# Performance work log

Measured on AMD Instinct MI355X. Metric: run time of the kernel, lower is better.

Reference implementation:

```python
import jax, jax.numpy as jnp
import numpy as np

E = 512          # embed_dim
H = 8            # num_heads
FF = 2048        # ff_dim
MAX_LEN = 5000   # DynamicPositionalEncoding max_len
LN_EPS = 1e-5


def _layernorm(x, g, b):
    mu = jnp.mean(x, axis=-1, keepdims=True)
    var = jnp.mean((x - mu) ** 2, axis=-1, keepdims=True)
    return (x - mu) / jnp.sqrt(var + LN_EPS) * g + b


def setup_inputs() -> dict:
    key = jax.random.key(0)
    ks = jax.random.split(key, 12)
    S, B = 2048, 4
    s = 0.02
    return {
        "x": jax.random.normal(ks[0], (S, B, E), dtype=jnp.float32),
        "pos": jnp.zeros((1, MAX_LEN, E), dtype=jnp.float32),  # torch init: zeros Parameter
        "in_proj_w": jax.random.normal(ks[1], (3 * E, E), dtype=jnp.float32) * s,
        "in_proj_b": jnp.zeros((3 * E,), dtype=jnp.float32),
        "out_w": jax.random.normal(ks[2], (E, E), dtype=jnp.float32) * s,
        "out_b": jnp.zeros((E,), dtype=jnp.float32),
        "w1": jax.random.normal(ks[3], (FF, E), dtype=jnp.float32) * s,
        "b1": jnp.zeros((FF,), dtype=jnp.float32),
        "w2": jax.random.normal(ks[4], (E, FF), dtype=jnp.float32) * s,
        "b2": jnp.zeros((E,), dtype=jnp.float32),
        "g1": jnp.ones((E,), dtype=jnp.float32),
        "be1": jnp.zeros((E,), dtype=jnp.float32),
        "g2": jnp.ones((E,), dtype=jnp.float32),
        "be2": jnp.zeros((E,), dtype=jnp.float32),
        "local_window_size": 128,
    }


def reference(x, pos, in_proj_w, in_proj_b, out_w, out_b, w1, b1, w2, b2,
              g1, be1, g2, be2, local_window_size):
    S, B, _ = x.shape
    w = int(local_window_size)
    # quirk of original: pos encoding sliced by x.size(1) == batch, broadcast over seq
    x = x + pos[:, :B, :]

    # additive mask: local window [i-w, i+w] allowed, plus global columns every 2w
    i = jnp.arange(S)[:, None]
    j = jnp.arange(S)[None, :]
    allowed = (jnp.abs(i - j) <= w) | (j % (2 * w) == 0)
    mask = jnp.where(allowed, 0.0, -jnp.inf).astype(x.dtype)  # (S, S)

    # multihead self-attention (torch MHA semantics, seq-first)
    qkv = x @ in_proj_w.T + in_proj_b                 # (S, B, 3E)
    q, k, v = jnp.split(qkv, 3, axis=-1)
    hd = E // H

    def heads(t):  # (S, B, E) -> (B, H, S, hd)
        return t.reshape(S, B, H, hd).transpose(1, 2, 0, 3)

    q, k, v = heads(q), heads(k), heads(v)
    scale = 1.0 / jnp.sqrt(jnp.asarray(hd, x.dtype))
    scores = jnp.einsum("bhqd,bhkd->bhqk", q * scale, k) + mask
    attn = jax.nn.softmax(scores, axis=-1)
    y = jnp.einsum("bhqk,bhkd->bhqd", attn, v)        # (B, H, S, hd)
    y = y.transpose(2, 0, 1, 3).reshape(S, B, E)
    attn_out = y @ out_w.T + out_b

    x = _layernorm(x + attn_out, g1, be1)
    ff = jax.nn.relu(x @ w1.T + b1) @ w2.T + b2
    x = _layernorm(x + ff, g2, be2)
    return x
```

## Files before the change

### kernel.cpp

```cpp
#include <hip/hip_runtime.h>
#include <hip/hip_bf16.h>
#include <math.h>

#define S_LEN 2048
#define B_SZ  4
#define E_DIM 512
#define H_NUM 8
#define HD    64
#define FF_DIM 2048
#define NROWS 8192
#define WIN   128

typedef unsigned short u16;
typedef __bf16 bf16x8 __attribute__((ext_vector_type(8)));
typedef float  f32x4  __attribute__((ext_vector_type(4)));

__device__ __forceinline__ u16 f2bf(float f) {
  union { float f; unsigned u; } v; v.f = f;
  unsigned u = v.u;
  return (u16)((u + 0x7fffu + ((u >> 16) & 1u)) >> 16);
}

__device__ __forceinline__ unsigned cvtpk(float lo, float hi) {
  unsigned r;
  asm("v_cvt_pk_bf16_f32 %0, %1, %2" : "=v"(r) : "v"(lo), "v"(hi));
  return r;
}

__device__ __forceinline__ void gl_lds16(const u16* gp, u16* lp) {
  __builtin_amdgcn_global_load_lds(
      (const __attribute__((address_space(1))) unsigned int*)gp,
      (__attribute__((address_space(3))) unsigned int*)lp, 16, 0, 0);
}

__global__ __launch_bounds__(256) void prep_kernel(
    const float* __restrict__ x, const float* __restrict__ pos,
    float* __restrict__ xp, u16* __restrict__ xpb,
    const float* __restrict__ s0, const float* __restrict__ s1,
    const float* __restrict__ s2, const float* __restrict__ s3,
    u16* __restrict__ d0, u16* __restrict__ d1,
    u16* __restrict__ d2, u16* __restrict__ d3) {
  int i = blockIdx.x * blockDim.x + threadIdx.x;
  if (i < 1048576) {
    float4 xv = ((const float4*)x)[i];
    float4 pv = ((const float4*)pos)[i & 511];
    float4 o;
    o.x = xv.x + pv.x; o.y = xv.y + pv.y; o.z = xv.z + pv.z; o.w = xv.w + pv.w;
    ((float4*)xp)[i] = o;
    ushort4 ob; ob.x = f2bf(o.x); ob.y = f2bf(o.y); ob.z = f2bf(o.z); ob.w = f2bf(o.w);
    ((ushort4*)xpb)[i] = ob;
  } else {
    int j = i - 1048576;
    const int n0 = 196608, n1 = 65536, n2 = 262144;
    const float4* sp; ushort4* dp; int off;
    if (j < n0)                { sp = (const float4*)s0; dp = (ushort4*)d0; off = j; }
    else if (j < n0 + n1)      { sp = (const float4*)s1; dp = (ushort4*)d1; off = j - n0; }
    else if (j < n0 + n1 + n2) { sp = (const float4*)s2; dp = (ushort4*)d2; off = j - n0 - n1; }
    else                       { sp = (const float4*)s3; dp = (ushort4*)d3; off = j - n0 - n1 - n2; }
    float4 v = sp[off];
    ushort4 o; o.x = f2bf(v.x); o.y = f2bf(v.y); o.z = f2bf(v.z); o.w = f2bf(v.w);
    dp[off] = o;
  }
}

#define GBK 64

template <int BN, int GY>
__global__ __launch_bounds__(256) void mfma_gemm(
    const u16* __restrict__ A, const u16* __restrict__ W,
    const float* __restrict__ bias, float* __restrict__ outf,
    u16* __restrict__ outb, int M, int N, int K, int mode,
    u16* __restrict__ qb, u16* __restrict__ kb, u16* __restrict__ vb) {
  constexpr int TJ = BN / 32;
  __shared__ u16 SMEM[2 * 128 * GBK + 2 * BN * GBK];
  u16* As0 = SMEM;
  u16* Bs0 = SMEM + 2 * 128 * GBK;
  int tid = threadIdx.x;
  int lane = tid & 63;
  int w = tid >> 6;
  int lin = blockIdx.y * 64 + blockIdx.x;
  int xcd = lin & 7, slot = lin >> 3;
  int jj = slot % GY;
  int mm = (slot / GY) * 8 + xcd;
  int m0 = mm * 128;
  int j0 = jj * BN;
  int wrow = (w >> 1) * 64;
  int wcol = (w & 1) * (BN / 2);
  int lm = lane & 15;
  int kq = lane >> 4;
  int sw = lm & 7;
  int r8 = lane >> 3;
  int csrc = ((lane & 7) ^ r8) << 3;

  f32x4 acc[4][TJ];
#pragma unroll
  for (int i = 0; i < 4; i++)
#pragma unroll
    for (int j = 0; j < TJ; j++) acc[i][j] = (f32x4){0.f, 0.f, 0.f, 0.f};

  const u16* Ab = A + (size_t)m0 * K;
  const u16* Wb = W + (size_t)j0 * K;

  size_t soff[4];
#pragma unroll
  for (int u = 0; u < 4; u++)
    soff[u] = (size_t)(u * 32 + w * 8 + r8) * K + csrc;

  auto stage = [&](int kt, int pb) {
#pragma unroll
    for (int u = 0; u < 4; u++)
      gl_lds16(&Ab[soff[u] + kt], &As0[pb * 128 * GBK + (u * 4 + w) * 512]);
#pragma unroll
    for (int u = 0; u < TJ; u++)
      gl_lds16(&Wb[soff[u] + kt], &Bs0[pb * BN * GBK + (u * 4 + w) * 512]);
  };

  stage(0, 0);
  int pb = 0;
  for (int kt = 0; kt < K; kt += GBK) {
    __syncthreads();
    if (kt + GBK < K) stage(kt + GBK, pb ^ 1);
#pragma unroll
    for (int k2 = 0; k2 < GBK; k2 += 32) {
      int cc = ((((k2 >> 3) + kq) ^ sw) << 3);
      bf16x8 af[4], bfr[TJ];
#pragma unroll
      for (int t = 0; t < 4; t++)
        af[t] = *(const bf16x8*)&As0[pb * 128 * GBK + (wrow + t * 16 + lm) * GBK + cc];
#pragma unroll
      for (int tj = 0; tj < TJ; tj++)
        bfr[tj] = *(const bf16x8*)&Bs0[pb * BN * GBK + (wcol + tj * 16 + lm) * GBK + cc];
#pragma unroll
      for (int ti = 0; ti < 4; ti++)
#pragma unroll
        for (int tj = 0; tj < TJ; tj++)
          acc[ti][tj] = __builtin_amdgcn_mfma_f32_16x16x32_bf16(
              af[ti], bfr[tj], acc[ti][tj], 0, 0, 0);
    }
    pb ^= 1;
  }

  __syncthreads();
  if (mode == 0) {
    float* Cf = (float*)SMEM;
    constexpr int CF = BN + 4;
#pragma unroll
    for (int p = 0; p < 2; p++) {
      if ((w >> 1) == p) {
#pragma unroll
        for (int tj = 0; tj < TJ; tj++) {
          float bv = bias[j0 + wcol + tj * 16 + lm];
#pragma unroll
          for (int ti = 0; ti < 4; ti++)
#pragma unroll
            for (int r = 0; r < 4; r++)
              Cf[(ti * 16 + kq * 4 + r) * CF + wcol + tj * 16 + lm] =
                  acc[ti][tj][r] + bv;
        }
      }
      __syncthreads();
      constexpr int RC4 = BN / 4;
#pragma unroll
      for (int it = 0; it < 64 * RC4 / 256; it++) {
        int id = it * 256 + tid;
        int row = id / RC4, c4 = (id % RC4) * 4;
        float4 vq = *(float4*)&Cf[row * CF + c4];
        *(float4*)&outf[(size_t)(m0 + p * 64 + row) * N + j0 + c4] = vq;
      }
      __syncthreads();
    }
  } else {
    u16* Cs = (u16*)SMEM;
    constexpr int CS = BN + 8;
#pragma unroll
    for (int tj = 0; tj < TJ; tj++) {
      int colj = j0 + wcol + tj * 16 + lm;
      float bv = bias[colj];
      float qs = (mode == 2 && colj < 512) ? 0.125f : 1.f;
#pragma unroll
      for (int ti = 0; ti < 4; ti++)
#pragma unroll
        for (int r = 0; r < 4; r++) {
          float val = acc[ti][tj][r] + bv;
          if (mode == 1) val = fmaxf(val, 0.f);
          Cs[(wrow + ti * 16 + kq * 4 + r) * CS + wcol + tj * 16 + lm] =
              f2bf(val * qs);
        }
    }
    __syncthreads();
    constexpr int RC8 = BN / 8;
#pragma unroll
    for (int it = 0; it < 128 * RC8 / 256; it++) {
      int id = it * 256 + tid;
      int row = id / RC8, c8 = (id % RC8) * 8;
      uint4 vq = *(uint4*)&Cs[row * CS + c8];
      if (mode == 1) {
        *(uint4*)&outb[(size_t)(m0 + row) * N + j0 + c8] = vq;
      } else {
        int col = j0 + c8;
        int which = col >> 9;
        int e = col & 511;
        int h = e >> 6, d0 = e & 63;
        int m = m0 + row, s = m >> 2, b = m & 3;
        u16* dst = (which == 0) ? qb : (which == 1) ? kb : vb;
        *(uint4*)&dst[((size_t)(b * H_NUM + h) * S_LEN + s) * HD + d0] = vq;
      }
    }
  }
}

__global__ __launch_bounds__(256) void vtrans_kernel(
    const u16* __restrict__ vb, u16* __restrict__ vt) {
  __shared__ u16 T[64 * 72];
  int tid = threadIdx.x;
  int bh = blockIdx.y, sc = blockIdx.x;
  const u16* src = vb + ((size_t)bh * S_LEN + sc * 64) * HD;
#pragma unroll
  for (int it = 0; it < 2; it++) {
    int id = it * 256 + tid;
    int srow = id >> 3, d8 = (id & 7) * 8;
    ushort4 v0 = *(const ushort4*)&src[srow * HD + d8];
    ushort4 v1 = *(const ushort4*)&src[srow * HD + d8 + 4];
    u16 arr[8] = {v0.x, v0.y, v0.z, v0.w, v1.x, v1.y, v1.z, v1.w};
#pragma unroll
    for (int j = 0; j < 8; j++) {
      int d = d8 + j;
      int rs = srow ^ (((d >> 3) & 7) << 3);
      T[d * 72 + rs] = arr[j];
    }
  }
  __syncthreads();
#pragma unroll
  for (int it = 0; it < 2; it++) {
    int id = it * 256 + tid;
    int d = id >> 3, s8 = (id & 7) * 8;
    int blk = (s8 >> 3) ^ ((d >> 3) & 7);
    uint4 vq = *(uint4*)&T[d * 72 + (blk << 3)];
    *(uint4*)&vt[((size_t)bh * HD + d) * S_LEN + sc * 64 + s8] = vq;
  }
}

__global__ __launch_bounds__(256) void attn_mfma_kernel(
    const u16* __restrict__ q, const u16* __restrict__ k,
    const u16* __restrict__ vt, u16* __restrict__ yb) {
  __shared__ u16 Ks[2 * 4096];
  __shared__ u16 Vs[2 * 4096];
  __shared__ u16 Ps[4096];
  int tid = threadIdx.x, lane = tid & 63, w = tid >> 6;
  int quad = lane >> 4, lm = lane & 15;
  int sw = lm & 7;
  int r8 = lane >> 3;
  int csrc = ((lane & 7) ^ r8) << 3;
  int lin = blockIdx.y * 32 + blockIdx.x;
  int xcd = lin & 7, slot = lin >> 3;
  int bh = xcd * 4 + (slot >> 5);
  int i0 = (slot & 31) * 64;
  int b = bh >> 3, h = bh & 7;
  const u16* qp = q + ((size_t)bh * S_LEN + i0) * HD;
  const u16* kp = k + (size_t)bh * S_LEN * HD;
  const u16* vp = vt + (size_t)bh * HD * S_LEN;

  bf16x8 qreg[2];
  {
    const u16* qr = qp + (size_t)(w * 16 + lm) * HD + quad * 8;
    qreg[0] = *(const bf16x8*)&qr[0];
    qreg[1] = *(const bf16x8*)&qr[32];
  }
  int psrow = (w * 16 + lm) * 64;
  int pshalf = (quad & 1) << 2;
  int psgq = quad >> 1;

  int cl = i0 - WIN; if (cl < 0) cl = 0;
  int chi = i0 + 63 + WIN; if (chi > S_LEN - 1) chi = S_LEN - 1;
  int nch = (chi - cl + 64) >> 6;
  int tlo = (cl + 255) >> 8;
  int thi0 = (chi >> 8) + 1;
  int ng = tlo + 8 - thi0;

  auto stage_local = [&](int ch, int pbuf) {
    int c0 = cl + (ch << 6);
#pragma unroll
    for (int u = 0; u < 2; u++) {
      int seg = u * 4 + w;
      int r = seg * 8 + r8;
      gl_lds16(&kp[(size_t)(c0 + r) * HD + csrc], &Ks[pbuf * 4096 + seg * 512]);
      gl_lds16(&vp[(size_t)r * S_LEN + c0 + csrc], &Vs[pbuf * 4096 + seg * 512]);
    }
  };
  auto stage_global = [&](int pbuf) {
    if (w == 0) {
      int rr = lane >> 3;
      int grow = (rr < tlo) ? (rr << 8) : ((thi0 + rr - tlo) << 8);
      if (rr >= ng) grow = 0;
      gl_lds16(&kp[(size_t)grow * HD + (((lane & 7) ^ rr) << 3)], &Ks[pbuf * 4096]);
    }
    for (int e = tid; e < 64 * 8; e += 256) {
      int d = e & 63, cg = e >> 6;
      if (cg < ng) {
        int gs = (cg < tlo) ? (cg << 8) : ((thi0 + cg - tlo) << 8);
        Vs[pbuf * 4096 + d * 64 + ((d & 7) << 3) + cg] = vp[(size_t)d * S_LEN + gs];
      }
    }
  };

  float m_i = -INFINITY, l_i = 0.f;
  f32x4 o[4];
#pragma unroll
  for (int tj = 0; tj < 4; tj++) o[tj] = (f32x4){0.f, 0.f, 0.f, 0.f};

  stage_local(0, 0);
  __syncthreads();
  int pb = 0;
  for (int ch = 0; ch < nch; ch++) {
    if (ch + 1 < nch) stage_local(ch + 1, pb ^ 1);
    else stage_global(pb ^ 1);

    f32x4 s[4];
#pragma unroll
    for (int tj = 0; tj < 4; tj++) s[tj] = (f32x4){0.f, 0.f, 0.f, 0.f};
    __builtin_amdgcn_s_setprio(1);
#pragma unroll
    for (int hh = 0; hh < 2; hh++) {
      int cb = (hh << 2) + quad;
      bf16x8 qf = qreg[hh];
#pragma unroll
      for (int tj = 0; tj < 4; tj++) {
        bf16x8 kf = *(const bf16x8*)&Ks[pb * 4096 + (tj * 16 + lm) * 64 + ((cb ^ sw) << 3)];
        s[tj] = __builtin_amdgcn_mfma_f32_16x16x32_bf16(kf, qf, s[tj], 0, 0, 0);
      }
    }
    __builtin_amdgcn_s_setprio(0);
    float mx = fmaxf(
        fmaxf(fmaxf(fmaxf(s[0][0], s[0][1]), fmaxf(s[0][2], s[0][3])),
              fmaxf(fmaxf(s[1][0], s[1][1]), fmaxf(s[1][2], s[1][3]))),
        fmaxf(fmaxf(fmaxf(s[2][0], s[2][1]), fmaxf(s[2][2], s[2][3])),
              fmaxf(fmaxf(s[3][0], s[3][1]), fmaxf(s[3][2], s[3][3]))));
    mx = fmaxf(mx, __shfl_xor(mx, 16));
    mx = fmaxf(mx, __shfl_xor(mx, 32));
    float mnew = fmaxf(m_i, mx);
    float al = __expf(m_i - mnew);
    float rs = 0.f;
#pragma unroll
    for (int tj = 0; tj < 4; tj++)
#pragma unroll
      for (int r = 0; r < 4; r++) {
        float p = __expf(s[tj][r] - mnew);
        s[tj][r] = p; rs += p;
      }
    rs += __shfl_xor(rs, 16);
    rs += __shfl_xor(rs, 32);
    l_i = l_i * al + rs;
    m_i = mnew;
#pragma unroll
    for (int tj = 0; tj < 4; tj++) {
      o[tj][0] *= al; o[tj][1] *= al; o[tj][2] *= al; o[tj][3] *= al;
    }
#pragma unroll
    for (int tj = 0; tj < 4; tj++) {
      uint2 up;
      up.x = cvtpk(s[tj][0], s[tj][1]);
      up.y = cvtpk(s[tj][2], s[tj][3]);
      *(uint2*)&Ps[psrow + ((((tj * 2 + psgq) ^ sw) << 3) | pshalf)] = up;
    }
    __builtin_amdgcn_s_setprio(1);
#pragma unroll
    for (int hh = 0; hh < 2; hh++) {
      int cb = (hh << 2) + quad;
      bf16x8 pf = *(const bf16x8*)&Ps[psrow + ((cb ^ sw) << 3)];
#pragma unroll
      for (int tj = 0; tj < 4; tj++) {
        bf16x8 vf = *(const bf16x8*)&Vs[pb * 4096 + (tj * 16 + lm) * 64 + ((cb ^ sw) << 3)];
        o[tj] = __builtin_amdgcn_mfma_f32_16x16x32_bf16(vf, pf, o[tj], 0, 0, 0);
      }
    }
    __builtin_amdgcn_s_setprio(0);
    __syncthreads();
    pb ^= 1;
  }

  {
    f32x4 s0 = (f32x4){0.f, 0.f, 0.f, 0.f};
#pragma unroll
    for (int hh = 0; hh < 2; hh++) {
      int cb = (hh << 2) + quad;
      bf16x8 kf = *(const bf16x8*)&Ks[pb * 4096 + lm * 64 + ((cb ^ sw) << 3)];
      s0 = __builtin_amdgcn_mfma_f32_16x16x32_bf16(kf, qreg[hh], s0, 0, 0, 0);
    }
#pragma unroll
    for (int r = 0; r < 4; r++)
      if (quad * 4 + r >= ng) s0[r] = -INFINITY;
    float mx = fmaxf(fmaxf(s0[0], s0[1]), fmaxf(s0[2], s0[3]));
    mx = fmaxf(mx, __shfl_xor(mx, 16));
    mx = fmaxf(mx, __shfl_xor(mx, 32));
    float mnew = fmaxf(m_i, mx);
    float al = __expf(m_i - mnew);
    float rs = 0.f;
#pragma unroll
    for (int r = 0; r < 4; r++) { float p = __expf(s0[r] - mnew); s0[r] = p; rs += p; }
    rs += __shfl_xor(rs, 16);
    rs += __shfl_xor(rs, 32);
    l_i = l_i * al + rs;
    m_i = mnew;
#pragma unroll
    for (int tj = 0; tj < 4; tj++) {
      o[tj][0] *= al; o[tj][1] *= al; o[tj][2] *= al; o[tj][3] *= al;
    }
    uint2 up;
    up.x = cvtpk(s0[0], s0[1]);
    up.y = cvtpk(s0[2], s0[3]);
    *(uint2*)&Ps[psrow + (((psgq ^ sw) << 3) | pshalf)] = up;
    *(uint2*)&Ps[psrow + ((((2 + psgq) ^ sw) << 3) | pshalf)] = (uint2){0u, 0u};
    bf16x8 pf = *(const bf16x8*)&Ps[psrow + ((quad ^ sw) << 3)];
#pragma unroll
    for (int tj = 0; tj < 4; tj++) {
      bf16x8 vf = *(const bf16x8*)&Vs[pb * 4096 + (tj * 16 + lm) * 64 + ((quad ^ sw) << 3)];
      o[tj] = __builtin_amdgcn_mfma_f32_16x16x32_bf16(vf, pf, o[tj], 0, 0, 0);
    }
  }

  float inv = 1.f / l_i;
#pragma unroll
  for (int tj = 0; tj < 4; tj++) {
    uint2 up;
    up.x = cvtpk(o[tj][0] * inv, o[tj][1] * inv);
    up.y = cvtpk(o[tj][2] * inv, o[tj][3] * inv);
    *(uint2*)&Ps[psrow + ((((tj * 2 + psgq) ^ sw) << 3) | pshalf)] = up;
  }
  __syncthreads();
#pragma unroll
  for (int it = 0; it < 2; it++) {
    int id = it * 256 + tid;
    int row = id >> 3, c8 = (id & 7) * 8;
    int blk = (id & 7) ^ (row & 7);
    uint4 vq = *(uint4*)&Ps[row * 64 + (blk << 3)];
    *(uint4*)&yb[((size_t)(i0 + row) * B_SZ + b) * E_DIM + h * HD + c8] = vq;
  }
}

__global__ __launch_bounds__(256) void add_ln_kernel(
    const float* __restrict__ a, const float* __restrict__ r,
    const float* __restrict__ g, const float* __restrict__ be,
    float* __restrict__ out, u16* __restrict__ outb) {
  int wave = threadIdx.x >> 6;
  int lane = threadIdx.x & 63;
  int row = blockIdx.x * 4 + wave;
  const float* ar = a + (size_t)row * E_DIM;
  const float* rr = r + (size_t)row * E_DIM;
  float vals[8];
  float s = 0.f;
#pragma unroll
  for (int t = 0; t < 8; t++) {
    vals[t] = ar[t * 64 + lane] + rr[t * 64 + lane];
    s += vals[t];
  }
#pragma unroll
  for (int o = 32; o >= 1; o >>= 1) s += __shfl_xor(s, o, 64);
  float mu = s * (1.f / E_DIM);
  float vs = 0.f;
#pragma unroll
  for (int t = 0; t < 8; t++) { float d = vals[t] - mu; vs += d * d; }
#pragma unroll
  for (int o = 32; o >= 1; o >>= 1) vs += __shfl_xor(vs, o, 64);
  float inv = rsqrtf(vs * (1.f / E_DIM) + 1e-5f);
  float* orow = out + (size_t)row * E_DIM;
  u16* obrow = outb ? outb + (size_t)row * E_DIM : nullptr;
#pragma unroll
  for (int t = 0; t < 8; t++) {
    int e = t * 64 + lane;
    float val = (vals[t] - mu) * inv * g[e] + be[e];
    orow[e] = val;
    if (obrow) obrow[e] = f2bf(val);
  }
}

extern "C" void kernel_launch(void* const* d_in, const int* in_sizes, int n_in,
                              void* d_out, int out_size, void* d_ws, size_t ws_size,
                              hipStream_t stream) {
  const float* x     = (const float*)d_in[0];
  const float* pos   = (const float*)d_in[1];
  const float* in_w  = (const float*)d_in[2];
  const float* in_b  = (const float*)d_in[3];
  const float* out_w = (const float*)d_in[4];
  const float* out_b = (const float*)d_in[5];
  const float* w1    = (const float*)d_in[6];
  const float* b1    = (const float*)d_in[7];
  const float* w2    = (const float*)d_in[8];
  const float* b2    = (const float*)d_in[9];
  const float* g1    = (const float*)d_in[10];
  const float* be1   = (const float*)d_in[11];
  const float* g2    = (const float*)d_in[12];
  const float* be2   = (const float*)d_in[13];
  float* out = (float*)d_out;

  char* base = (char*)d_ws;
  float* xp    = (float*)(base);
  u16*   xpb   = (u16*)(base + ((size_t)16 << 20));
  u16*   qb    = (u16*)(base + ((size_t)24 << 20));
  u16*   kb    = (u16*)(base + ((size_t)32 << 20));
  u16*   vb    = (u16*)(base + ((size_t)40 << 20));
  u16*   ybf   = (u16*)(base + ((size_t)48 << 20));
  float* aprj  = (float*)(base + ((size_t)56 << 20));
  u16*   vt    = (u16*)(base + ((size_t)56 << 20));
  u16*   inwb  = (u16*)(base + ((size_t)72 << 20));
  u16*   outwb = (u16*)(base + ((size_t)74 << 20));
  u16*   w1b   = (u16*)(base + ((size_t)76 << 20));
  u16*   w2b   = (u16*)(base + ((size_t)78 << 20));
  float* x1    = xp;
  u16*   x1b   = xpb;
  u16*   ff1b  = qb;
  float* ff2   = aprj;

  prep_kernel<<<7168, 256, 0, stream>>>(x, pos, xp, xpb,
                                        in_w, out_w, w1, w2, inwb, outwb, w1b, w2b);
  mfma_gemm<128, 12><<<dim3(64, 12), 256, 0, stream>>>(xpb, inwb, in_b, nullptr, nullptr,
                                                       NROWS, 1536, 512, 2, qb, kb, vb);
  vtrans_kernel<<<dim3(32, 32), 256, 0, stream>>>(vb, vt);
  attn_mfma_kernel<<<dim3(32, 32), 256, 0, stream>>>(qb, kb, vt, ybf);
  mfma_gemm<64, 8><<<dim3(64, 8), 256, 0, stream>>>(ybf, outwb, out_b, aprj, nullptr,
                                                    NROWS, 512, 512, 0, nullptr, nullptr, nullptr);
  add_ln_kernel<<<2048, 256, 0, stream>>>(xp, aprj, g1, be1, x1, x1b);
  mfma_gemm<128, 16><<<dim3(64, 16), 256, 0, stream>>>(x1b, w1b, b1, nullptr, ff1b,
                                                       NROWS, 2048, 512, 1, nullptr, nullptr, nullptr);
  mfma_gemm<64, 8><<<dim3(64, 8), 256, 0, stream>>>(ff1b, w2b, b2, ff2, nullptr,
                                                    NROWS, 512, 2048, 0, nullptr, nullptr, nullptr);
  add_ln_kernel<<<2048, 256, 0, stream>>>(x1, ff2, g2, be2, out, nullptr);
}
```

Baseline: 227.6 us.

## Add triple-buffered LDS pipeline to GEMM and retile FF1 to 64-wide blocks

Adds a DEPTH template parameter to the MFMA GEMM. The new three-buffer LDS path keeps two global-to-LDS tile loads in flight and waits with an explicit vmcnt count instead of draining everything each iteration. The out-projection and both FFN GEMMs switch to the 3-deep pipeline, and FF1 moves from BN=128 to BN=64 tiles with twice as many column blocks. This aims to hide global load latency and raise occupancy, at the cost of more LDS per block and, for FF1, more re-reading of the A operand.

```diff
diff --git a/kernel.cpp b/kernel.cpp
--- a/kernel.cpp
+++ b/kernel.cpp
@@ -65,16 +65,16 @@
 
 #define GBK 64
 
-template <int BN, int GY>
+template <int BN, int GY, int DEPTH>
 __global__ __launch_bounds__(256) void mfma_gemm(
     const u16* __restrict__ A, const u16* __restrict__ W,
     const float* __restrict__ bias, float* __restrict__ outf,
     u16* __restrict__ outb, int M, int N, int K, int mode,
     u16* __restrict__ qb, u16* __restrict__ kb, u16* __restrict__ vb) {
   constexpr int TJ = BN / 32;
-  __shared__ u16 SMEM[2 * 128 * GBK + 2 * BN * GBK];
-  u16* As0 = SMEM;
-  u16* Bs0 = SMEM + 2 * 128 * GBK;
+  constexpr int NLD = 4 + TJ;
+  constexpr int BSZ = (128 + BN) * GBK;
+  __shared__ u16 SMEM[DEPTH * BSZ];
   int tid = threadIdx.x;
   int lane = tid & 63;
   int w = tid >> 6;
@@ -106,38 +106,87 @@
   for (int u = 0; u < 4; u++)
     soff[u] = (size_t)(u * 32 + w * 8 + r8) * K + csrc;
 
-  auto stage = [&](int kt, int pb) {
-#pragma unroll
-    for (int u = 0; u < 4; u++)
-      gl_lds16(&Ab[soff[u] + kt], &As0[pb * 128 * GBK + (u * 4 + w) * 512]);
-#pragma unroll
-    for (int u = 0; u < TJ; u++)
-      gl_lds16(&Wb[soff[u] + kt], &Bs0[pb * BN * GBK + (u * 4 + w) * 512]);
-  };
-
-  stage(0, 0);
-  int pb = 0;
-  for (int kt = 0; kt < K; kt += GBK) {
-    __syncthreads();
-    if (kt + GBK < K) stage(kt + GBK, pb ^ 1);
-#pragma unroll
-    for (int k2 = 0; k2 < GBK; k2 += 32) {
-      int cc = ((((k2 >> 3) + kq) ^ sw) << 3);
-      bf16x8 af[4], bfr[TJ];
-#pragma unroll
-      for (int t = 0; t < 4; t++)
-        af[t] = *(const bf16x8*)&As0[pb * 128 * GBK + (wrow + t * 16 + lm) * GBK + cc];
-#pragma unroll
-      for (int tj = 0; tj < TJ; tj++)
-        bfr[tj] = *(const bf16x8*)&Bs0[pb * BN * GBK + (wcol + tj * 16 + lm) * GBK + cc];
-#pragma unroll
-      for (int ti = 0; ti < 4; ti++)
+  if constexpr (DEPTH == 2) {
+    u16* As0 = SMEM;
+    u16* Bs0 = SMEM + 2 * 128 * GBK;
+    auto stage = [&](int kt, int pbb) {
+#pragma unroll
+      for (int u = 0; u < 4; u++)
+        gl_lds16(&Ab[soff[u] + kt], &As0[pbb * 128 * GBK + (u * 4 + w) * 512]);
+#pragma unroll
+      for (int u = 0; u < TJ; u++)
+        gl_lds16(&Wb[soff[u] + kt], &Bs0[pbb * BN * GBK + (u * 4 + w) * 512]);
+    };
+    stage(0, 0);
+    int pb = 0;
+    for (int kt = 0; kt < K; kt += GBK) {
+      __syncthreads();
+      if (kt + GBK < K) stage(kt + GBK, pb ^ 1);
+#pragma unroll
+      for (int k2 = 0; k2 < GBK; k2 += 32) {
+        int cc = ((((k2 >> 3) + kq) ^ sw) << 3);
+        bf16x8 af[4], bfr[TJ];
+#pragma unroll
+        for (int t = 0; t < 4; t++)
+          af[t] = *(const bf16x8*)&As0[pb * 128 * GBK + (wrow + t * 16 + lm) * GBK + cc];
 #pragma unroll
         for (int tj = 0; tj < TJ; tj++)
-          acc[ti][tj] = __builtin_amdgcn_mfma_f32_16x16x32_bf16(
-              af[ti], bfr[tj], acc[ti][tj], 0, 0, 0);
-    }
-    pb ^= 1;
+          bfr[tj] = *(const bf16x8*)&Bs0[pb * BN * GBK + (wcol + tj * 16 + lm) * GBK + cc];
+#pragma unroll
+        for (int ti = 0; ti < 4; ti++)
+#pragma unroll
+          for (int tj = 0; tj < TJ; tj++)
+            acc[ti][tj] = __builtin_amdgcn_mfma_f32_16x16x32_bf16(
+                af[ti], bfr[tj], acc[ti][tj], 0, 0, 0);
+      }
+      pb ^= 1;
+    }
+  } else {
+    auto stage3 = [&](int kt, int b) {
+      u16* base = &SMEM[b * BSZ];
+#pragma unroll
+      for (int u = 0; u < 4; u++)
+        gl_lds16(&Ab[soff[u] + kt], &base[(u * 4 + w) * 512]);
+#pragma unroll
+      for (int u = 0; u < TJ; u++)
+        gl_lds16(&Wb[soff[u] + kt], &base[128 * GBK + (u * 4 + w) * 512]);
+    };
+    const int T = K / GBK;
+    stage3(0, 0);
+    stage3(GBK, 1);
+    int cur = 0;
+    for (int t = 0; t < T; ++t) {
+      if (t + 1 < T) {
+        asm volatile("s_waitcnt vmcnt(%0)" :: "n"(NLD) : "memory");
+      } else {
+        asm volatile("s_waitcnt vmcnt(0)" ::: "memory");
+      }
+      __builtin_amdgcn_s_barrier();
+      if (t + 2 < T) {
+        int nb = cur + 2; if (nb >= 3) nb -= 3;
+        stage3((t + 2) * GBK, nb);
+      }
+      const u16* As = &SMEM[cur * BSZ];
+      const u16* Bs = &SMEM[cur * BSZ + 128 * GBK];
+#pragma unroll
+      for (int k2 = 0; k2 < GBK; k2 += 32) {
+        int cc = ((((k2 >> 3) + kq) ^ sw) << 3);
+        bf16x8 af[4], bfr[TJ];
+#pragma unroll
+        for (int t2 = 0; t2 < 4; t2++)
+          af[t2] = *(const bf16x8*)&As[(wrow + t2 * 16 + lm) * GBK + cc];
+#pragma unroll
+        for (int tj = 0; tj < TJ; tj++)
+          bfr[tj] = *(const bf16x8*)&Bs[(wcol + tj * 16 + lm) * GBK + cc];
+#pragma unroll
+        for (int ti = 0; ti < 4; ti++)
+#pragma unroll
+          for (int tj = 0; tj < TJ; tj++)
+            acc[ti][tj] = __builtin_amdgcn_mfma_f32_16x16x32_bf16(
+                af[ti], bfr[tj], acc[ti][tj], 0, 0, 0);
+      }
+      cur = (cur == 2) ? 0 : cur + 1;
+    }
   }
 
   __syncthreads();
@@ -512,16 +561,16 @@
 
   prep_kernel<<<7168, 256, 0, stream>>>(x, pos, xp, xpb,
                                         in_w, out_w, w1, w2, inwb, outwb, w1b, w2b);
-  mfma_gemm<128, 12><<<dim3(64, 12), 256, 0, stream>>>(xpb, inwb, in_b, nullptr, nullptr,
-                                                       NROWS, 1536, 512, 2, qb, kb, vb);
+  mfma_gemm<128, 12, 2><<<dim3(64, 12), 256, 0, stream>>>(xpb, inwb, in_b, nullptr, nullptr,
+                                                          NROWS, 1536, 512, 2, qb, kb, vb);
   vtrans_kernel<<<dim3(32, 32), 256, 0, stream>>>(vb, vt);
   attn_mfma_kernel<<<dim3(32, 32), 256, 0, stream>>>(qb, kb, vt, ybf);
-  mfma_gemm<64, 8><<<dim3(64, 8), 256, 0, stream>>>(ybf, outwb, out_b, aprj, nullptr,
-                                                    NROWS, 512, 512, 0, nullptr, nullptr, nullptr);
+  mfma_gemm<64, 8, 3><<<dim3(64, 8), 256, 0, stream>>>(ybf, outwb, out_b, aprj, nullptr,
+                                                       NROWS, 512, 512, 0, nullptr, nullptr, nullptr);
   add_ln_kernel<<<2048, 256, 0, stream>>>(xp, aprj, g1, be1, x1, x1b);
-  mfma_gemm<128, 16><<<dim3(64, 16), 256, 0, stream>>>(x1b, w1b, b1, nullptr, ff1b,
-                                                       NROWS, 2048, 512, 1, nullptr, nullptr, nullptr);
-  mfma_gemm<64, 8><<<dim3(64, 8), 256, 0, stream>>>(ff1b, w2b, b2, ff2, nullptr,
-                                                    NROWS, 512, 2048, 0, nullptr, nullptr, nullptr);
+  mfma_gemm<64, 32, 3><<<dim3(64, 32), 256, 0, stream>>>(x1b, w1b, b1, nullptr, ff1b,
+                                                         NROWS, 2048, 512, 1, nullptr, nullptr, nullptr);
+  mfma_gemm<64, 8, 3><<<dim3(64, 8), 256, 0, stream>>>(ff1b, w2b, b2, ff2, nullptr,
+                                                       NROWS, 512, 2048, 0, nullptr, nullptr, nullptr);
   add_ln_kernel<<<2048, 256, 0, stream>>>(x1, ff2, g2, be2, out, nullptr);
 }
```

New measurement: 230.9 us. Within noise of the previous version (+1.4%).
